# Kernel optimization log

Hardware: AMD Instinct MI355X
Metric: run time of the kernel (lower is better)

Reference implementation:

```python
import jax, jax.numpy as jnp
import numpy as np

N = 100000      # nodes
D = 128         # embed_dim == hidden_size (code forces them equal)
M = 3           # edge_types / meta-paths
L = 2           # layers
E = 1600000     # edges per meta-path (avg degree 16)
ATT = 128       # semantic attention hidden size


def setup_inputs():
    key = jax.random.key(0)
    ks = jax.random.split(key, 8)
    x = jnp.arange(N)
    edge_index0 = jax.random.randint(ks[0], (2, E), 0, N)
    edge_index1 = jax.random.randint(ks[1], (2, E), 0, N)
    edge_index2 = jax.random.randint(ks[2], (2, E), 0, N)
    embed_table = jax.random.normal(ks[3], (N, D), dtype=jnp.float32) * 0.02
    W = jax.random.normal(ks[4], (L, M, D, D), dtype=jnp.float32) / np.sqrt(D)
    B = jnp.zeros((L, M, D), dtype=jnp.float32)
    att_w1 = jax.random.normal(ks[5], (L, D, ATT), dtype=jnp.float32) / np.sqrt(D)
    att_b1 = jnp.zeros((L, ATT), dtype=jnp.float32)
    att_w2 = jax.random.normal(ks[6], (L, ATT, 1), dtype=jnp.float32) / np.sqrt(ATT)
    return dict(x=x, edge_index0=edge_index0, edge_index1=edge_index1,
                edge_index2=edge_index2, embed_table=embed_table, W=W, B=B,
                att_w1=att_w1, att_b1=att_b1, att_w2=att_w2)


def _gcn_conv(h, W, b, src, dst):
    # GCNConv(normalize=True): self-loops already appended to src/dst.
    deg = jax.ops.segment_sum(jnp.ones_like(dst, dtype=h.dtype), dst, num_segments=N)
    dinv = jnp.where(deg > 0, jax.lax.rsqrt(deg), 0.0)
    norm = dinv[src] * dinv[dst]                       # [E+N]
    hw = h @ W                                         # [N, D]
    msg = hw[src] * norm[:, None]                      # gather + scale
    return jax.ops.segment_sum(msg, dst, num_segments=N) + b


def reference(x, edge_index0, edge_index1, edge_index2,
              embed_table, W, B, att_w1, att_b1, att_w2):
    edges = [edge_index0, edge_index1, edge_index2]
    loops = jnp.arange(N)
    srcs = [jnp.concatenate([e[0], loops]) for e in edges]
    dsts = [jnp.concatenate([e[1], loops]) for e in edges]

    h = embed_table[x]                                 # [N, D]
    for l in range(L):
        sems = [_gcn_conv(h, W[l, m], B[l, m], srcs[m], dsts[m]) for m in range(M)]
        z = jnp.stack(sems, axis=1)                    # [N, M, D]
        # semantic attention: Linear -> tanh -> Linear(no bias), softmax over M
        w = jnp.tanh(z @ att_w1[l] + att_b1[l]) @ att_w2[l]   # [N, M, 1]
        beta = jax.nn.softmax(w, axis=1)
        h = (beta * z).sum(axis=1)                     # [N, D]
    return jax.nn.log_softmax(h, axis=1)
```

## Files before the change

kernel.cpp:

```cpp
#include <hip/hip_runtime.h>
#include <hip/hip_bf16.h>

#define NN 100000
#define DD 128
#define MM 3
#define EE 1600000
#define NBUK ((NN + 127) / 128)
#define CAP 2336
#define CSRTOT ((size_t)NBUK * CAP)
#define TILE_E 2048
#define NTILES ((EE + TILE_E - 1) / TILE_E)
#define TH_PITCH 784
#define HSCALE 64.0f
#define HINV (1.0f / 64.0f)

typedef unsigned int uint32_hip;
typedef short short8 __attribute__((ext_vector_type(8)));
typedef float floatx4 __attribute__((ext_vector_type(4)));
typedef float floatx2 __attribute__((ext_vector_type(2)));

__device__ __forceinline__ float bf2f(short s) {
  return __uint_as_float(((uint32_hip)(unsigned short)s) << 16);
}
__device__ __forceinline__ unsigned short f2bf(float f) {
  union { __hip_bfloat16 b; unsigned short u; } cv;
  cv.b = __float2bfloat16(f);
  return cv.u;
}
__device__ __forceinline__ uint32_hip packbf2(float x, float y) {
  return (uint32_hip)f2bf(x) | ((uint32_hip)f2bf(y) << 16);
}
__device__ __forceinline__ float tanh_apx(float x) {
  float e = __expf(2.0f * x);
  return 1.0f - 2.0f / (e + 1.0f);
}
__device__ __forceinline__ uint32_hip pack_fp8x4(float a, float b, float c, float d) {
  uint32_hip w = 0;
  w = __builtin_amdgcn_cvt_pk_fp8_f32(a, b, w, false);
  w = __builtin_amdgcn_cvt_pk_fp8_f32(c, d, w, true);
  return w;
}
__device__ __forceinline__ float h2f(uint32_hip u) {
  union { unsigned short us; _Float16 h; } cv;
  cv.us = (unsigned short)u;
  return (float)cv.h;
}
__device__ __forceinline__ unsigned short f2h(float f) {
  union { unsigned short us; _Float16 h; } cv;
  cv.h = (_Float16)f;
  return cv.us;
}
__device__ __forceinline__ void dec8(uint2 hv, float* f) {
  floatx2 p0 = __builtin_amdgcn_cvt_pk_f32_fp8((int)hv.x, false);
  floatx2 p1 = __builtin_amdgcn_cvt_pk_f32_fp8((int)hv.x, true);
  floatx2 p2 = __builtin_amdgcn_cvt_pk_f32_fp8((int)hv.y, false);
  floatx2 p3 = __builtin_amdgcn_cvt_pk_f32_fp8((int)hv.y, true);
  f[0] = p0.x; f[1] = p0.y; f[2] = p1.x; f[3] = p1.y;
  f[4] = p2.x; f[5] = p2.y; f[6] = p3.x; f[7] = p3.y;
}

__global__ __launch_bounds__(256) void hist_kernel(const int* __restrict__ e0,
                                                   const int* __restrict__ e1,
                                                   const int* __restrict__ e2,
                                                   int* __restrict__ thist) {
  __shared__ int hist[NBUK];
  int m = blockIdx.y, tile = blockIdx.x, t = threadIdx.x;
  const int* ei = (m == 0) ? e0 : (m == 1) ? e1 : e2;
  const int* dst = ei + EE;
  int beg = tile * TILE_E, end = min(beg + TILE_E, EE);
  for (int b = t; b < NBUK; b += 256) hist[b] = 0;
  __syncthreads();
  for (int e = beg + t; e < end; e += 256) atomicAdd(&hist[dst[e] >> 7], 1);
  __syncthreads();
  int* th = thist + (size_t)m * NBUK * TH_PITCH + tile;
  for (int b = t; b < NBUK; b += 256) th[(size_t)b * TH_PITCH] = hist[b];
}

__global__ __launch_bounds__(256) void scan_kernel(int* __restrict__ thist,
                                                   int* __restrict__ bcur) {
  __shared__ int sw[256];
  int b = blockIdx.x, m = blockIdx.y, t = threadIdx.x;
  int* th = thist + ((size_t)m * NBUK + b) * TH_PITCH;
  int v[4];
  int s = 0;
#pragma unroll
  for (int j = 0; j < 4; ++j) {
    int tt = t * 4 + j;
    v[j] = (tt < NTILES) ? th[tt] : 0;
    s += v[j];
  }
  sw[t] = s;
  __syncthreads();
  for (int off = 1; off < 256; off <<= 1) {
    int u = (t >= off) ? sw[t - off] : 0;
    __syncthreads();
    sw[t] += u;
    __syncthreads();
  }
  int base = b * CAP + sw[t] - s;
#pragma unroll
  for (int j = 0; j < 4; ++j) {
    int tt = t * 4 + j;
    if (tt < NTILES) th[tt] = base;
    base += v[j];
  }
  if (t == 255) bcur[m * NBUK + b] = b * CAP + sw[255];
}

__global__ __launch_bounds__(256) void scatter_kernel(const int* __restrict__ e0,
                                                      const int* __restrict__ e1,
                                                      const int* __restrict__ e2,
                                                      const int* __restrict__ thist,
                                                      uint32_hip* __restrict__ ebuf) {
  __shared__ int cur[NBUK];
  int m = blockIdx.y, tile = blockIdx.x, t = threadIdx.x;
  const int* ei = (m == 0) ? e0 : (m == 1) ? e1 : e2;
  const int* dst = ei + EE;
  int beg = tile * TILE_E, end = min(beg + TILE_E, EE);
  const int* th = thist + (size_t)m * NBUK * TH_PITCH + tile;
  for (int b = t; b < NBUK; b += 256) cur[b] = th[(size_t)b * TH_PITCH];
  __syncthreads();
  uint32_hip* eb = ebuf + (size_t)m * CSRTOT;
  for (int e = beg + t; e < end; e += 256) {
    int d = dst[e];
    int pos = atomicAdd(&cur[d >> 7], 1);
    eb[pos] = (uint32_hip)ei[e] | ((uint32_hip)(d & 127) << 17);
  }
}

__global__ void bucket_sort_kernel(uint32_hip* __restrict__ ebuf, const int* __restrict__ bcur,
                                   int* __restrict__ astart, unsigned short* __restrict__ sdeg) {
  __shared__ uint32_hip ebl[CAP];
  __shared__ int cnt[128];
  __shared__ int pos[128];
  int m = blockIdx.y, b = blockIdx.x, t = threadIdx.x;
  int base = b * CAP;
  int ct = bcur[m * NBUK + b] - base;
  uint32_hip* eb = ebuf + (size_t)m * CSRTOT + base;
  for (int e = t; e < ct; e += 256) ebl[e] = eb[e];
  if (t < 128) cnt[t] = 0;
  __syncthreads();
  for (int e = t; e < ct; e += 256) atomicAdd(&cnt[ebl[e] >> 17], 1);
  __syncthreads();
  if (t < 128) pos[t] = cnt[t];
  __syncthreads();
  for (int off = 1; off < 128; off <<= 1) {
    int v = (t < 128 && t >= off) ? pos[t - off] : 0;
    __syncthreads();
    if (t < 128) pos[t] += v;
    __syncthreads();
  }
  int node0 = b * 128;
  if (t < 128) {
    int excl = pos[t] - cnt[t];
    pos[t] = excl;
    int node = node0 + t;
    if (node < NN) {
      astart[(size_t)m * NN + node] = base + excl;
      sdeg[(size_t)m * NN + node] = (unsigned short)cnt[t];
    }
  }
  __syncthreads();
  for (int e = t; e < ct; e += 256) {
    uint32_hip p = ebl[e];
    int q = atomicAdd(&pos[p >> 17], 1);
    eb[q] = p & 0x1FFFFu;
  }
}

__global__ void norm_embed_kernel(uint32_hip* __restrict__ ebuf, const int* __restrict__ bcur,
                                  const unsigned short* __restrict__ sdeg) {
  int m = blockIdx.y, b = blockIdx.x, t = threadIdx.x;
  int base = b * CAP;
  int ct = bcur[m * NBUK + b] - base;
  uint32_hip* eb = ebuf + (size_t)m * CSRTOT + base;
  const unsigned short* sd = sdeg + (size_t)m * NN;
  for (int e = t; e < ct; e += 256) {
    uint32_hip s = eb[e] & 0x1FFFFu;
    float dv = rsqrtf((float)(sd[s] + 1));
    eb[e] = s | ((uint32_hip)f2h(dv) << 17);
  }
}

__global__ void embed_kernel(const int* __restrict__ x, const float* __restrict__ tbl,
                             uint32_hip* __restrict__ hq) {
  int i = blockIdx.x * 256 + threadIdx.x;
  if (i < NN * 32) {
    int n = i >> 5;
    int c = i & 31;
    float4 v = ((const float4*)tbl)[(size_t)x[n] * 32 + c];
    hq[(size_t)n * 32 + c] =
        pack_fp8x4(v.x * HSCALE, v.y * HSCALE, v.z * HSCALE, v.w * HSCALE);
  }
}

__global__ __launch_bounds__(256) void agg_kernel(const uint32_hip* __restrict__ hq,
                                                  const unsigned short* __restrict__ sdeg,
                                                  const int* __restrict__ astart,
                                                  const uint32_hip* __restrict__ csr,
                                                  uint32_hip* __restrict__ zall) {
  int m = blockIdx.y;
  const unsigned short* sd = sdeg + (size_t)m * NN;
  const int* as_ = astart + (size_t)m * NN;
  const uint32_hip* cs = csr + (size_t)m * CSRTOT;
  uint32_hip* zo = zall + (size_t)m * NN * 64;
  int t = threadIdx.x;
  int wave = t >> 6, lane = t & 63;
  int g = lane >> 4, l = lane & 15;
  int n = blockIdx.x * 16 + wave * 4 + g;
  int deg = sd[n];
  float di = rsqrtf((float)(deg + 1));

  float ac[8];
  {
    uint2 hv = *(const uint2*)(hq + (size_t)n * 32 + l * 2);
    float f[8];
    dec8(hv, f);
#pragma unroll
    for (int j = 0; j < 8; ++j) ac[j] = di * f[j];
  }

  int e = as_[n];
  int end = e + deg;
  bool v0 = e < end, v1 = (e + 1) < end;
  uint32_hip c0 = cs[v0 ? e : 0];
  uint32_hip c1 = cs[v1 ? e + 1 : 0];
  while (__any(v0)) {
    int en = e + 2;
    bool u0 = en < end, u1 = (en + 1) < end;
    uint32_hip d0 = cs[u0 ? en : 0];
    uint32_hip d1 = cs[u1 ? en + 1 : 0];
    float n0 = v0 ? h2f(c0 >> 17) : 0.f;
    float n1 = v1 ? h2f(c1 >> 17) : 0.f;
    int s0 = c0 & 0x1FFFF, s1 = c1 & 0x1FFFF;
    uint2 h0 = *(const uint2*)(hq + (size_t)s0 * 32 + l * 2);
    uint2 h1 = *(const uint2*)(hq + (size_t)s1 * 32 + l * 2);
    float f0[8], f1[8];
    dec8(h0, f0);
    dec8(h1, f1);
#pragma unroll
    for (int j = 0; j < 8; ++j) ac[j] = fmaf(n0, f0[j], ac[j]);
#pragma unroll
    for (int j = 0; j < 8; ++j) ac[j] = fmaf(n1, f1[j], ac[j]);
    e = en;
    v0 = u0;
    v1 = u1;
    c0 = d0;
    c1 = d1;
  }

  float sc = di * HINV;
  uint4 w;
  w.x = packbf2(ac[0] * sc, ac[1] * sc);
  w.y = packbf2(ac[2] * sc, ac[3] * sc);
  w.z = packbf2(ac[4] * sc, ac[5] * sc);
  w.w = packbf2(ac[6] * sc, ac[7] * sc);
  *(uint4*)(zo + (size_t)n * 64 + l * 4) = w;
}

__global__ __launch_bounds__(256) void mfma_gemm_kernel(unsigned short* __restrict__ zall,
                                                        const float* __restrict__ Wall,
                                                        const float* __restrict__ Ball) {
  __shared__ unsigned short Wt[128 * 136];
  int m = blockIdx.y;
  const float* Wmat = Wall + (size_t)m * DD * DD;
  const float* bias = Ball + (size_t)m * DD;
  unsigned short* Z = zall + (size_t)m * NN * DD;
  int t = threadIdx.x;
  {
    uint32_hip* Wt_u = (uint32_hip*)Wt;
#pragma unroll
    for (int i = 0; i < 32; ++i) {
      int idx = i * 256 + t;
      int k2 = idx >> 7;
      int nn = idx & 127;
      float w0 = Wmat[(2 * k2) * 128 + nn];
      float w1 = Wmat[(2 * k2 + 1) * 128 + nn];
      Wt_u[nn * 68 + k2] = packbf2(w0, w1);
    }
  }
  __syncthreads();
  int wave = t >> 6, lane = t & 63;
  int quad = lane >> 4, ln = lane & 15;
  int rowbase = blockIdx.x * 64 + wave * 16;
  int arow = rowbase + ln;
  int arowc = (arow < NN) ? arow : (NN - 1);
  const short8* zrow = (const short8*)(Z + (size_t)arowc * 128);
  floatx4 acc[8];
#pragma unroll
  for (int c = 0; c < 8; ++c) acc[c] = (floatx4){0.f, 0.f, 0.f, 0.f};
#pragma unroll
  for (int kt = 0; kt < 4; ++kt) {
    short8 a = zrow[kt * 4 + quad];
#pragma unroll
    for (int c = 0; c < 8; ++c) {
      const short8* bp = (const short8*)(Wt + (c * 16 + ln) * 136 + kt * 32 + quad * 8);
      acc[c] = __builtin_amdgcn_mfma_f32_16x16x32_bf16(a, *bp, acc[c], 0, 0, 0);
    }
  }
#pragma unroll
  for (int c = 0; c < 8; ++c) {
    int col = c * 16 + ln;
    float bs = bias[col];
#pragma unroll
    for (int r = 0; r < 4; ++r) {
      int grow = rowbase + quad * 4 + r;
      if (grow < NN) Z[(size_t)grow * 128 + col] = f2bf(acc[c][r] + bs);
    }
  }
}

__global__ __launch_bounds__(256) void att_combine_kernel(
    const unsigned short* __restrict__ Z, const float* __restrict__ W1,
    const float* __restrict__ b1, const float* __restrict__ w2,
    uint32_hip* __restrict__ hq, float* __restrict__ fout, int last) {
  __shared__ unsigned short Wt[128 * 136];
  __shared__ float sc[4][3][16];
  int t = threadIdx.x;
  {
    uint32_hip* Wt_u = (uint32_hip*)Wt;
#pragma unroll
    for (int i = 0; i < 32; ++i) {
      int idx = i * 256 + t;
      int k2 = idx >> 7;
      int nn = idx & 127;
      float w0 = W1[(2 * k2) * 128 + nn];
      float w1 = W1[(2 * k2 + 1) * 128 + nn];
      Wt_u[nn * 68 + k2] = packbf2(w0, w1);
    }
  }
  __syncthreads();
  int wave = t >> 6, lane = t & 63;
  int quad = lane >> 4, ln = lane & 15;
  int nodebase = blockIdx.x * 64 + wave * 16;
  int frow = nodebase + ln;
  int frowc = (frow < NN) ? frow : (NN - 1);
  short8 af[3][4];
#pragma unroll
  for (int m = 0; m < 3; ++m) {
    const short8* zr = (const short8*)(Z + ((size_t)m * NN + frowc) * 128);
#pragma unroll
    for (int kt = 0; kt < 4; ++kt) af[m][kt] = zr[kt * 4 + quad];
  }
#pragma unroll
  for (int m = 0; m < 3; ++m) {
    floatx4 acc[8];
#pragma unroll
    for (int c = 0; c < 8; ++c) acc[c] = (floatx4){0.f, 0.f, 0.f, 0.f};
#pragma unroll
    for (int kt = 0; kt < 4; ++kt) {
#pragma unroll
      for (int c = 0; c < 8; ++c) {
        const short8* bp = (const short8*)(Wt + (c * 16 + ln) * 136 + kt * 32 + quad * 8);
        acc[c] = __builtin_amdgcn_mfma_f32_16x16x32_bf16(af[m][kt], *bp, acc[c], 0, 0, 0);
      }
    }
    float rows[4] = {0.f, 0.f, 0.f, 0.f};
#pragma unroll
    for (int c = 0; c < 8; ++c) {
      int col = c * 16 + ln;
      float bb = b1[col];
      float ww = w2[col];
#pragma unroll
      for (int r = 0; r < 4; ++r) rows[r] += tanh_apx(acc[c][r] + bb) * ww;
    }
#pragma unroll
    for (int off = 8; off > 0; off >>= 1) {
#pragma unroll
      for (int r = 0; r < 4; ++r) rows[r] += __shfl_down(rows[r], off);
    }
    if (ln == 0) {
#pragma unroll
      for (int r = 0; r < 4; ++r) sc[wave][m][quad * 4 + r] = rows[r];
    }
  }
  __syncthreads();
  float s0 = sc[wave][0][ln], s1 = sc[wave][1][ln], s2 = sc[wave][2][ln];
  float mx = fmaxf(s0, fmaxf(s1, s2));
  float e0 = __expf(s0 - mx), e1 = __expf(s1 - mx), e2 = __expf(s2 - mx);
  float inv = 1.0f / (e0 + e1 + e2);
  float bb0 = e0 * inv, bb1 = e1 * inv, bb2 = e2 * inv;
  float o[4][8];
#pragma unroll
  for (int kt = 0; kt < 4; ++kt) {
#pragma unroll
    for (int j = 0; j < 8; ++j) {
      o[kt][j] = bb0 * bf2f(af[0][kt][j]) + bb1 * bf2f(af[1][kt][j]) + bb2 * bf2f(af[2][kt][j]);
    }
  }
  if (!last) {
    if (frow < NN) {
#pragma unroll
      for (int kt = 0; kt < 4; ++kt) {
        uint2 v;
        v.x = pack_fp8x4(o[kt][0] * HSCALE, o[kt][1] * HSCALE, o[kt][2] * HSCALE,
                         o[kt][3] * HSCALE);
        v.y = pack_fp8x4(o[kt][4] * HSCALE, o[kt][5] * HSCALE, o[kt][6] * HSCALE,
                         o[kt][7] * HSCALE);
        *(uint2*)&hq[(size_t)frow * 32 + kt * 8 + quad * 2] = v;
      }
    }
  } else {
    float vmx = o[0][0];
#pragma unroll
    for (int kt = 0; kt < 4; ++kt)
#pragma unroll
      for (int j = 0; j < 8; ++j) vmx = fmaxf(vmx, o[kt][j]);
    vmx = fmaxf(vmx, __shfl_xor(vmx, 16));
    vmx = fmaxf(vmx, __shfl_xor(vmx, 32));
    float ss = 0.f;
#pragma unroll
    for (int kt = 0; kt < 4; ++kt)
#pragma unroll
      for (int j = 0; j < 8; ++j) ss += __expf(o[kt][j] - vmx);
    ss += __shfl_xor(ss, 16);
    ss += __shfl_xor(ss, 32);
    float lse = vmx + logf(ss);
    if (frow < NN) {
#pragma unroll
      for (int kt = 0; kt < 4; ++kt) {
        float4 a, b;
        a.x = o[kt][0] - lse; a.y = o[kt][1] - lse; a.z = o[kt][2] - lse; a.w = o[kt][3] - lse;
        b.x = o[kt][4] - lse; b.y = o[kt][5] - lse; b.z = o[kt][6] - lse; b.w = o[kt][7] - lse;
        float* dst = fout + (size_t)frow * 128 + kt * 32 + quad * 8;
        *(float4*)dst = a;
        *(float4*)(dst + 4) = b;
      }
    }
  }
}

extern "C" void kernel_launch(void* const* d_in, const int* in_sizes, int n_in,
                              void* d_out, int out_size, void* d_ws, size_t ws_size,
                              hipStream_t stream) {
  const int* x = (const int*)d_in[0];
  const int* e0 = (const int*)d_in[1];
  const int* e1 = (const int*)d_in[2];
  const int* e2 = (const int*)d_in[3];
  const float* embed = (const float*)d_in[4];
  const float* W = (const float*)d_in[5];
  const float* B = (const float*)d_in[6];
  const float* aw1 = (const float*)d_in[7];
  const float* ab1 = (const float*)d_in[8];
  const float* aw2 = (const float*)d_in[9];
  float* out = (float*)d_out;
  uint32_hip* hq = (uint32_hip*)d_out;

  char* ws = (char*)d_ws;
  size_t off = 0;
  auto alloc = [&](size_t bytes) {
    void* p = ws + off;
    off += (bytes + 255) & ~(size_t)255;
    return p;
  };
  unsigned short* z = (unsigned short*)alloc((size_t)MM * NN * DD * 2);
  uint32_hip* ebuf = (uint32_hip*)alloc((size_t)MM * CSRTOT * 4);
  int* astart = (int*)alloc((size_t)MM * NN * 4);
  unsigned short* sdeg = (unsigned short*)alloc((size_t)MM * NN * 2);
  int* bcur = (int*)alloc((size_t)MM * NBUK * 4);
  int* thist = (int*)alloc((size_t)MM * NBUK * TH_PITCH * 4);

  dim3 bs(256);
  hist_kernel<<<dim3(NTILES, 3), bs, 0, stream>>>(e0, e1, e2, thist);
  scan_kernel<<<dim3(NBUK, 3), bs, 0, stream>>>(thist, bcur);
  scatter_kernel<<<dim3(NTILES, 3), bs, 0, stream>>>(e0, e1, e2, thist, ebuf);
  bucket_sort_kernel<<<dim3(NBUK, 3), bs, 0, stream>>>(ebuf, bcur, astart, sdeg);
  norm_embed_kernel<<<dim3(NBUK, 3), bs, 0, stream>>>(ebuf, bcur, sdeg);
  embed_kernel<<<dim3((NN * 32 + 255) / 256), bs, 0, stream>>>(x, embed, hq);

  for (int l = 0; l < 2; ++l) {
    agg_kernel<<<dim3((NN + 15) / 16, 3), bs, 0, stream>>>(
        (const uint32_hip*)hq, sdeg, astart, ebuf, (uint32_hip*)z);
    mfma_gemm_kernel<<<dim3((NN + 63) / 64, 3), bs, 0, stream>>>(
        z, W + (size_t)l * 3 * DD * DD, B + (size_t)l * 3 * DD);
    att_combine_kernel<<<dim3((NN + 63) / 64), bs, 0, stream>>>(
        z, aw1 + (size_t)l * DD * DD, ab1 + (size_t)l * DD, aw2 + (size_t)l * DD, hq, out, l == 1);
  }
}
```

Baseline: 733.0 us.

## Restructure CSR build into coarser 512-node chunks with LDS-staged scatter

```diff
diff --git a/kernel.cpp b/kernel.cpp
--- a/kernel.cpp
+++ b/kernel.cpp
@@ -5,12 +5,12 @@
 #define DD 128
 #define MM 3
 #define EE 1600000
-#define NBUK ((NN + 127) / 128)
-#define CAP 2336
-#define CSRTOT ((size_t)NBUK * CAP)
-#define TILE_E 2048
+#define CH_NODES 512
+#define NC ((NN + CH_NODES - 1) / CH_NODES)
+#define ECAP 8960
+#define ECHTOT ((size_t)NC * ECAP)
+#define TILE_E 8192
 #define NTILES ((EE + TILE_E - 1) / TILE_E)
-#define TH_PITCH 784
 #define HSCALE 64.0f
 #define HINV (1.0f / 64.0f)
 
@@ -59,37 +59,30 @@
   f[4] = p2.x; f[5] = p2.y; f[6] = p3.x; f[7] = p3.y;
 }
 
-__global__ __launch_bounds__(256) void hist_kernel(const int* __restrict__ e0,
-                                                   const int* __restrict__ e1,
-                                                   const int* __restrict__ e2,
-                                                   int* __restrict__ thist) {
-  __shared__ int hist[NBUK];
+__global__ __launch_bounds__(256) void hist1_kernel(const int* __restrict__ e0,
+                                                    const int* __restrict__ e1,
+                                                    const int* __restrict__ e2,
+                                                    int* __restrict__ thist) {
+  __shared__ int hist[NC];
   int m = blockIdx.y, tile = blockIdx.x, t = threadIdx.x;
   const int* ei = (m == 0) ? e0 : (m == 1) ? e1 : e2;
   const int* dst = ei + EE;
   int beg = tile * TILE_E, end = min(beg + TILE_E, EE);
-  for (int b = t; b < NBUK; b += 256) hist[b] = 0;
-  __syncthreads();
-  for (int e = beg + t; e < end; e += 256) atomicAdd(&hist[dst[e] >> 7], 1);
-  __syncthreads();
-  int* th = thist + (size_t)m * NBUK * TH_PITCH + tile;
-  for (int b = t; b < NBUK; b += 256) th[(size_t)b * TH_PITCH] = hist[b];
-}
-
-__global__ __launch_bounds__(256) void scan_kernel(int* __restrict__ thist,
-                                                   int* __restrict__ bcur) {
+  if (t < NC) hist[t] = 0;
+  __syncthreads();
+  for (int e = beg + t; e < end; e += 256) atomicAdd(&hist[dst[e] >> 9], 1);
+  __syncthreads();
+  int* th = thist + (size_t)m * NC * NTILES + tile;
+  if (t < NC) th[(size_t)t * NTILES] = hist[t];
+}
+
+__global__ __launch_bounds__(256) void scan1_kernel(int* __restrict__ thist,
+                                                    int* __restrict__ ccount) {
   __shared__ int sw[256];
-  int b = blockIdx.x, m = blockIdx.y, t = threadIdx.x;
-  int* th = thist + ((size_t)m * NBUK + b) * TH_PITCH;
-  int v[4];
-  int s = 0;
-#pragma unroll
-  for (int j = 0; j < 4; ++j) {
-    int tt = t * 4 + j;
-    v[j] = (tt < NTILES) ? th[tt] : 0;
-    s += v[j];
-  }
-  sw[t] = s;
+  int c = blockIdx.x, m = blockIdx.y, t = threadIdx.x;
+  int* th = thist + ((size_t)m * NC + c) * NTILES;
+  int v = (t < NTILES) ? th[t] : 0;
+  sw[t] = v;
   __syncthreads();
   for (int off = 1; off < 256; off <<= 1) {
     int u = (t >= off) ? sw[t - off] : 0;
@@ -97,67 +90,105 @@
     sw[t] += u;
     __syncthreads();
   }
-  int base = b * CAP + sw[t] - s;
-#pragma unroll
-  for (int j = 0; j < 4; ++j) {
-    int tt = t * 4 + j;
-    if (tt < NTILES) th[tt] = base;
-    base += v[j];
-  }
-  if (t == 255) bcur[m * NBUK + b] = b * CAP + sw[255];
-}
-
-__global__ __launch_bounds__(256) void scatter_kernel(const int* __restrict__ e0,
-                                                      const int* __restrict__ e1,
-                                                      const int* __restrict__ e2,
-                                                      const int* __restrict__ thist,
-                                                      uint32_hip* __restrict__ ebuf) {
-  __shared__ int cur[NBUK];
+  if (t < NTILES) th[t] = c * ECAP + sw[t] - v;
+  if (t == NTILES - 1) ccount[m * NC + c] = sw[t];
+}
+
+__global__ __launch_bounds__(256) void scatter1_kernel(const int* __restrict__ e0,
+                                                       const int* __restrict__ e1,
+                                                       const int* __restrict__ e2,
+                                                       const int* __restrict__ thist,
+                                                       const int* __restrict__ ccount,
+                                                       uint32_hip* __restrict__ lvl1) {
+  __shared__ int gbase[NC];
+  __shared__ int spos[NC];
+  __shared__ int cur[NC];
+  __shared__ int sw[256];
+  __shared__ uint32_hip sval[TILE_E];
+  __shared__ unsigned char sbuk[TILE_E];
   int m = blockIdx.y, tile = blockIdx.x, t = threadIdx.x;
   const int* ei = (m == 0) ? e0 : (m == 1) ? e1 : e2;
   const int* dst = ei + EE;
+  const int* th = thist + (size_t)m * NC * NTILES + tile;
+  int cnt = 0;
+  if (t < NC) {
+    int gb = th[(size_t)t * NTILES];
+    int gn = (tile + 1 < NTILES) ? th[(size_t)t * NTILES + 1] : t * ECAP + ccount[m * NC + t];
+    gbase[t] = gb;
+    cnt = gn - gb;
+  }
+  sw[t] = cnt;
+  __syncthreads();
+  for (int off = 1; off < 256; off <<= 1) {
+    int u = (t >= off) ? sw[t - off] : 0;
+    __syncthreads();
+    sw[t] += u;
+    __syncthreads();
+  }
+  if (t < NC) {
+    spos[t] = sw[t] - cnt;
+    cur[t] = sw[t] - cnt;
+  }
+  __syncthreads();
   int beg = tile * TILE_E, end = min(beg + TILE_E, EE);
-  const int* th = thist + (size_t)m * NBUK * TH_PITCH + tile;
-  for (int b = t; b < NBUK; b += 256) cur[b] = th[(size_t)b * TH_PITCH];
-  __syncthreads();
-  uint32_hip* eb = ebuf + (size_t)m * CSRTOT;
+  int ct = end - beg;
   for (int e = beg + t; e < end; e += 256) {
-    int d = dst[e];
-    int pos = atomicAdd(&cur[d >> 7], 1);
-    eb[pos] = (uint32_hip)ei[e] | ((uint32_hip)(d & 127) << 17);
-  }
-}
-
-__global__ void bucket_sort_kernel(uint32_hip* __restrict__ ebuf, const int* __restrict__ bcur,
-                                   int* __restrict__ astart, unsigned short* __restrict__ sdeg) {
-  __shared__ uint32_hip ebl[CAP];
-  __shared__ int cnt[128];
-  __shared__ int pos[128];
-  int m = blockIdx.y, b = blockIdx.x, t = threadIdx.x;
-  int base = b * CAP;
-  int ct = bcur[m * NBUK + b] - base;
-  uint32_hip* eb = ebuf + (size_t)m * CSRTOT + base;
+    int s = ei[e], d = dst[e];
+    int b = d >> 9;
+    int r = atomicAdd(&cur[b], 1);
+    sval[r] = (uint32_hip)s | ((uint32_hip)(d & 511) << 17);
+    sbuk[r] = (unsigned char)b;
+  }
+  __syncthreads();
+  uint32_hip* eb = lvl1 + (size_t)m * ECHTOT;
+  for (int i = t; i < ct; i += 256) {
+    int b = sbuk[i];
+    eb[gbase[b] + (i - spos[b])] = sval[i];
+  }
+}
+
+__global__ __launch_bounds__(256) void sort2_kernel(uint32_hip* __restrict__ lvl1,
+                                                    const int* __restrict__ ccount,
+                                                    int* __restrict__ astart,
+                                                    unsigned short* __restrict__ sdeg) {
+  __shared__ uint32_hip ebl[ECAP];
+  __shared__ int cnt[CH_NODES];
+  __shared__ int pos[CH_NODES];
+  __shared__ int sw[256];
+  int m = blockIdx.y, c = blockIdx.x, t = threadIdx.x;
+  int base = c * ECAP;
+  int ct = ccount[m * NC + c];
+  uint32_hip* eb = lvl1 + (size_t)m * ECHTOT + base;
   for (int e = t; e < ct; e += 256) ebl[e] = eb[e];
-  if (t < 128) cnt[t] = 0;
+  cnt[t] = 0;
+  cnt[t + 256] = 0;
   __syncthreads();
   for (int e = t; e < ct; e += 256) atomicAdd(&cnt[ebl[e] >> 17], 1);
   __syncthreads();
-  if (t < 128) pos[t] = cnt[t];
-  __syncthreads();
-  for (int off = 1; off < 128; off <<= 1) {
-    int v = (t < 128 && t >= off) ? pos[t - off] : 0;
+  int c0 = cnt[2 * t], c1 = cnt[2 * t + 1];
+  int s = c0 + c1;
+  sw[t] = s;
+  __syncthreads();
+  for (int off = 1; off < 256; off <<= 1) {
+    int u = (t >= off) ? sw[t - off] : 0;
     __syncthreads();
-    if (t < 128) pos[t] += v;
+    sw[t] += u;
     __syncthreads();
   }
-  int node0 = b * 128;
-  if (t < 128) {
-    int excl = pos[t] - cnt[t];
-    pos[t] = excl;
-    int node = node0 + t;
-    if (node < NN) {
-      astart[(size_t)m * NN + node] = base + excl;
-      sdeg[(size_t)m * NN + node] = (unsigned short)cnt[t];
+  int excl = sw[t] - s;
+  pos[2 * t] = excl;
+  pos[2 * t + 1] = excl + c0;
+  int node0 = c * CH_NODES;
+  {
+    int n0 = node0 + 2 * t;
+    if (n0 < NN) {
+      astart[(size_t)m * NN + n0] = base + excl;
+      sdeg[(size_t)m * NN + n0] = (unsigned short)c0;
+    }
+    int n1 = node0 + 2 * t + 1;
+    if (n1 < NN) {
+      astart[(size_t)m * NN + n1] = base + excl + c0;
+      sdeg[(size_t)m * NN + n1] = (unsigned short)c1;
     }
   }
   __syncthreads();
@@ -168,12 +199,12 @@
   }
 }
 
-__global__ void norm_embed_kernel(uint32_hip* __restrict__ ebuf, const int* __restrict__ bcur,
+__global__ void norm_embed_kernel(uint32_hip* __restrict__ lvl1, const int* __restrict__ ccount,
                                   const unsigned short* __restrict__ sdeg) {
-  int m = blockIdx.y, b = blockIdx.x, t = threadIdx.x;
-  int base = b * CAP;
-  int ct = bcur[m * NBUK + b] - base;
-  uint32_hip* eb = ebuf + (size_t)m * CSRTOT + base;
+  int m = blockIdx.y, c = blockIdx.x, t = threadIdx.x;
+  int base = c * ECAP;
+  int ct = ccount[m * NC + c];
+  uint32_hip* eb = lvl1 + (size_t)m * ECHTOT + base;
   const unsigned short* sd = sdeg + (size_t)m * NN;
   for (int e = t; e < ct; e += 256) {
     uint32_hip s = eb[e] & 0x1FFFFu;
@@ -202,7 +233,7 @@
   int m = blockIdx.y;
   const unsigned short* sd = sdeg + (size_t)m * NN;
   const int* as_ = astart + (size_t)m * NN;
-  const uint32_hip* cs = csr + (size_t)m * CSRTOT;
+  const uint32_hip* cs = csr + (size_t)m * ECHTOT;
   uint32_hip* zo = zall + (size_t)m * NN * 64;
   int t = threadIdx.x;
   int wave = t >> 6, lane = t & 63;
@@ -454,23 +485,23 @@
     return p;
   };
   unsigned short* z = (unsigned short*)alloc((size_t)MM * NN * DD * 2);
-  uint32_hip* ebuf = (uint32_hip*)alloc((size_t)MM * CSRTOT * 4);
+  uint32_hip* lvl1 = (uint32_hip*)alloc((size_t)MM * ECHTOT * 4);
   int* astart = (int*)alloc((size_t)MM * NN * 4);
   unsigned short* sdeg = (unsigned short*)alloc((size_t)MM * NN * 2);
-  int* bcur = (int*)alloc((size_t)MM * NBUK * 4);
-  int* thist = (int*)alloc((size_t)MM * NBUK * TH_PITCH * 4);
+  int* ccount = (int*)alloc((size_t)MM * NC * 4);
+  int* thist = (int*)alloc((size_t)MM * NC * NTILES * 4);
 
   dim3 bs(256);
-  hist_kernel<<<dim3(NTILES, 3), bs, 0, stream>>>(e0, e1, e2, thist);
-  scan_kernel<<<dim3(NBUK, 3), bs, 0, stream>>>(thist, bcur);
-  scatter_kernel<<<dim3(NTILES, 3), bs, 0, stream>>>(e0, e1, e2, thist, ebuf);
-  bucket_sort_kernel<<<dim3(NBUK, 3), bs, 0, stream>>>(ebuf, bcur, astart, sdeg);
-  norm_embed_kernel<<<dim3(NBUK, 3), bs, 0, stream>>>(ebuf, bcur, sdeg);
+  hist1_kernel<<<dim3(NTILES, 3), bs, 0, stream>>>(e0, e1, e2, thist);
+  scan1_kernel<<<dim3(NC, 3), bs, 0, stream>>>(thist, ccount);
+  scatter1_kernel<<<dim3(NTILES, 3), bs, 0, stream>>>(e0, e1, e2, thist, ccount, lvl1);
+  sort2_kernel<<<dim3(NC, 3), bs, 0, stream>>>(lvl1, ccount, astart, sdeg);
+  norm_embed_kernel<<<dim3(NC, 3), bs, 0, stream>>>(lvl1, ccount, sdeg);
   embed_kernel<<<dim3((NN * 32 + 255) / 256), bs, 0, stream>>>(x, embed, hq);
 
   for (int l = 0; l < 2; ++l) {
     agg_kernel<<<dim3((NN + 15) / 16, 3), bs, 0, stream>>>(
-        (const uint32_hip*)hq, sdeg, astart, ebuf, (uint32_hip*)z);
+        (const uint32_hip*)hq, sdeg, astart, lvl1, (uint32_hip*)z);
     mfma_gemm_kernel<<<dim3((NN + 63) / 64, 3), bs, 0, stream>>>(
         z, W + (size_t)l * 3 * DD * DD, B + (size_t)l * 3 * DD);
     att_combine_kernel<<<dim3((NN + 63) / 64), bs, 0, stream>>>(
```

Result: faster. 650.7 us (-11.2%).
